# Kernel tuning notes

Measured on AMD Instinct MI355X. Metric: run time of the kernel, lower is better.

The kernel has to match this reference:

```python
import jax, jax.numpy as jnp
import numpy as np

B, C_IN, H, W = 8, 3, 256, 256
CH = 64          # encoder_channels
MSG_LEN = 30     # message_length
WM_R = 4         # watermark_radius
LP_R = 50        # low-pass filter radius


def _wm_positions(h, w, c, r, msg_len):
    # Replicates the nested-loop index ordering of apply_tree_ring_watermark.
    cy, cx = h // 2, w // 2
    ch, rr, cc = [], [], []
    idx = 0
    for chan in range(c):
        for i in range(-r, r + 1):
            for j in range(-r, r + 1):
                if idx >= msg_len:
                    break
                if not (0 <= cy + i < h and 0 <= cx + j < w):
                    continue
                if (i * i + j * j) ** 0.5 <= r:
                    ch.append(chan); rr.append(cy + i); cc.append(cx + j)
                    idx += 1
    return (np.asarray(ch, np.int32), np.asarray(rr, np.int32), np.asarray(cc, np.int32))

_WM_CH, _WM_ROW, _WM_COL = _wm_positions(H, W, CH, WM_R, MSG_LEN)


def conv2d(x, w, b, pad):
    y = jax.lax.conv_general_dilated(x, w, (1, 1), [(pad, pad), (pad, pad)],
                                     dimension_numbers=('NCHW', 'OIHW', 'NCHW'))
    return y + b[None, :, None, None]


def conv_bn_relu(x, w, b, g, be):
    y = conv2d(x, w, b, 1)
    m = y.mean(axis=(0, 2, 3), keepdims=True)
    v = y.var(axis=(0, 2, 3), keepdims=True)
    y = (y - m) * jax.lax.rsqrt(v + 1e-5) * g[None, :, None, None] + be[None, :, None, None]
    return jax.nn.relu(y)


def low_pass_filter(image, radius=LP_R):
    # np.fft per-channel low pass with a circular mask (cv2.circle disk), clip+uint8, /255.
    h, w = image.shape[-2:]
    yy = jnp.arange(h, dtype=jnp.float32) - h // 2
    xx = jnp.arange(w, dtype=jnp.float32) - w // 2
    mask = (yy[:, None] ** 2 + xx[None, :] ** 2) <= float(radius * radius)
    f = jnp.fft.fftshift(jnp.fft.fft2(image), axes=(-2, -1))
    low = jnp.fft.ifft2(jnp.fft.ifftshift(f * mask, axes=(-2, -1))).real
    low = jnp.floor(jnp.clip(low, 0.0, 255.0)) / 255.0  # uint8 cast = floor for non-neg
    # torch version detaches to CPU numpy -> no gradient through this path
    return jax.lax.stop_gradient(low.astype(image.dtype))


def apply_tree_ring_watermark(image_fft, message):
    # Vectorized replacement of the quadruple nested loop: fixed static scatter positions.
    vals = jax.lax.stop_gradient(message).astype(image_fft.dtype) * (1.0 + 1.0j)  # [B, L]
    return image_fft.at[:, _WM_CH, _WM_ROW, _WM_COL].set(vals)


def setup_inputs() -> dict:
    key = jax.random.key(0)
    ks = jax.random.split(key, 8)
    s = 0.05
    return {
        'image': jax.random.uniform(ks[0], (B, C_IN, H, W), jnp.float32) * 255.0,
        'message': jax.random.randint(ks[1], (B, MSG_LEN), 0, 2).astype(jnp.float32),
        'w0': jax.random.normal(ks[2], (CH, C_IN, 3, 3), jnp.float32) * s,
        'b0': jnp.zeros((CH,), jnp.float32),
        'g0': jnp.ones((CH,), jnp.float32),
        'be0': jnp.zeros((CH,), jnp.float32),
        'ws': jax.random.normal(ks[3], (3, CH, CH, 3, 3), jnp.float32) * s,
        'bs': jnp.zeros((3, CH), jnp.float32),
        'gs': jnp.ones((3, CH), jnp.float32),
        'bes': jnp.zeros((3, CH), jnp.float32),
        'acw': jax.random.normal(ks[4], (CH, CH + C_IN + MSG_LEN, 3, 3), jnp.float32) * s,
        'acb': jnp.zeros((CH,), jnp.float32),
        'acg': jnp.ones((CH,), jnp.float32),
        'acbe': jnp.zeros((CH,), jnp.float32),
        'fw': jax.random.normal(ks[5], (3, CH, 1, 1), jnp.float32) * s,
        'fb': jnp.zeros((3,), jnp.float32),
    }


def reference(image, message, w0, b0, g0, be0, ws, bs, gs, bes,
              acw, acb, acg, acbe, fw, fb):
    lp = low_pass_filter(image)
    x = conv_bn_relu(lp, w0, b0, g0, be0)
    for k in range(3):  # encoder_blocks - 1
        x = conv_bn_relu(x, ws[k], bs[k], gs[k], bes[k])
    f = jnp.fft.fft2(x)
    f = apply_tree_ring_watermark(f, message)
    enc = jnp.fft.ifft2(f).real
    msg_exp = jnp.broadcast_to(message[:, :, None, None], (B, MSG_LEN, H, W))
    concat = jnp.concatenate([msg_exp, enc, image], axis=1)
    y = conv_bn_relu(concat, acw, acb, acg, acbe)
    return conv2d(y, fw, fb, 0)
```

## Files before the change

kernel.cpp:

```cpp
#include <hip/hip_runtime.h>
#include <math.h>


#define NPX 65536
typedef unsigned short u16;
typedef __bf16 bfrag_t __attribute__((ext_vector_type(8)));
typedef float f32x4 __attribute__((ext_vector_type(4)));

__constant__ int WM_R_[30] = {124, 125,125,125,125,125, 126,126,126,126,126,126,126,
                              127,127,127,127,127,127,127,
                              128,128,128,128,128,128,128,128,128, 129};
__constant__ int WM_C_[30] = {128, 126,127,128,129,130, 125,126,127,128,129,130,131,
                              125,126,127,128,129,130,131,
                              124,125,126,127,128,129,130,131,132, 125};

__device__ __forceinline__ float bfu2f(unsigned int bits) {
    return __uint_as_float(bits << 16);
}
__device__ __forceinline__ u16 f2bu(float f) {
    unsigned int u = __float_as_uint(f);
    u += 0x7fffu + ((u >> 16) & 1u);
    return (u16)(u >> 16);
}

__global__ void k_tables(float* __restrict__ tw, float* __restrict__ d2t,
                         double* __restrict__ twd64) {
    int idx = blockIdx.x * 256 + threadIdx.x;
    if (idx < 256) {
        double ang = -2.0 * M_PI * (double)idx / 256.0;
        tw[idx]       = (float)cos(ang);
        tw[256 + idx] = (float)sin(ang);
        twd64[idx]       = cos(ang);
        twd64[256 + idx] = sin(ang);
    }
    int q = idx - 256;
    if (q >= 0 && q < 256 * 101) {
        int d = q / 101, kxi = q - d * 101;
        int vx = (kxi <= 50) ? kxi : kxi - 101;
        int r2 = 2500 - vx * vx;
        int L = 0;
        while ((L + 1) * (L + 1) <= r2) L++;
        double s = 1.0;
        for (int v = 1; v <= L; v++) s += 2.0 * cos(2.0 * M_PI * (double)(v * d) / 256.0);
        d2t[kxi * 256 + d] = (float)(s / 256.0);
    }
}

__global__ __launch_bounds__(256) void k_lp1(const float* __restrict__ img,
        const double* __restrict__ twd64, float* __restrict__ Y) {
    __shared__ double rowd[4][256];
    int y0 = blockIdx.x * 4, ch = blockIdx.y, tid = threadIdx.x;
#pragma unroll
    for (int r = 0; r < 4; r++)
        rowd[r][tid] = (double)img[ch * NPX + (y0 + r) * 256 + tid];
    __syncthreads();
    int kxi = tid & 127, rg = tid >> 7;
    if (kxi >= 101) return;
    int kx = (kxi <= 50) ? kxi : kxi + 155;
    double cr = twd64[kx], ci = twd64[256 + kx];
    double wr = 1.0, wi = 0.0;
    double a0r = 0, a0i = 0, a1r = 0, a1i = 0;
    const double* r0 = rowd[2 * rg];
    const double* r1 = rowd[2 * rg + 1];
    for (int x = 0; x < 256; x++) {
        double v0 = r0[x], v1 = r1[x];
        a0r += v0 * wr; a0i += v0 * wi;
        a1r += v1 * wr; a1i += v1 * wi;
        double t = wr * cr - wi * ci;
        wi = wr * ci + wi * cr;
        wr = t;
    }
    int y = y0 + 2 * rg;
    int o = ((kxi * 24 + ch) * 256 + y) * 2;
    Y[o]     = (float)a0r; Y[o + 1] = (float)a0i;
    Y[o + 2] = (float)a1r; Y[o + 3] = (float)a1i;
}

__global__ __launch_bounds__(256) void k_lp2(const float* __restrict__ Y,
        const float* __restrict__ d2t, float* __restrict__ W) {
    __shared__ double Ys[4][256][2];
    __shared__ double Dc[256];
    int kxi = blockIdx.x, chg = blockIdx.y, tid = threadIdx.x;
    const float* src = Y + (size_t)(kxi * 24 + chg * 4) * 512;
    double* ysf = (double*)Ys;
    for (int i = tid; i < 2048; i += 256) ysf[i] = (double)src[i];
    Dc[tid] = (double)d2t[kxi * 256 + tid];
    __syncthreads();
    int cs = tid >> 6, y4 = tid & 63;
    double wr[4] = {0, 0, 0, 0}, wi[4] = {0, 0, 0, 0};
    for (int yp = 0; yp < 256; yp++) {
        double yr = Ys[cs][yp][0], yi = Ys[cs][yp][1];
        double D0 = Dc[(y4 - yp) & 255];
        double D1 = Dc[(y4 + 64 - yp) & 255];
        double D2 = Dc[(y4 + 128 - yp) & 255];
        double D3 = Dc[(y4 + 192 - yp) & 255];
        wr[0] += D0 * yr; wi[0] += D0 * yi;
        wr[1] += D1 * yr; wi[1] += D1 * yi;
        wr[2] += D2 * yr; wi[2] += D2 * yi;
        wr[3] += D3 * yr; wi[3] += D3 * yi;
    }
    int ch = chg * 4 + cs;
#pragma unroll
    for (int k = 0; k < 4; k++) {
        int y = y4 + 64 * k;
        int o = ((ch * 256 + y) * 101 + kxi) * 2;
        W[o] = (float)wr[k]; W[o + 1] = (float)wi[k];
    }
}

__global__ __launch_bounds__(256) void k_lp3(const float* __restrict__ W,
        const double* __restrict__ twd64, float* __restrict__ lp) {
    __shared__ double wsr[101], wsi[101];
    int y = blockIdx.x, ch = blockIdx.y, x = threadIdx.x;
    if (x < 101) {
        int kxi = (x < 50) ? (x + 51) : (x - 50);
        wsr[x] = (double)W[((ch * 256 + y) * 101 + kxi) * 2];
        wsi[x] = (double)W[((ch * 256 + y) * 101 + kxi) * 2 + 1];
    }
    __syncthreads();
    int t0 = (50 * x) & 255;
    double wr = twd64[t0], wi = -twd64[256 + t0];
    double cr = twd64[x], ci = twd64[256 + x];
    double acc = 0.0;
    for (int j = 0; j < 101; j++) {
        acc += wsr[j] * wr + wsi[j] * wi;
        double t = wr * cr - wi * ci;
        wi = wr * ci + wi * cr;
        wr = t;
    }
    acc *= (1.0 / 256.0);
    acc = floor(fmin(fmax(acc, 0.0), 255.0)) / 255.0;
    lp[ch * NPX + y * 256 + x] = (float)acc;
}

__global__ __launch_bounds__(256, 2) void k_conv1(
    const float* __restrict__ lp, const float* __restrict__ w0,
    u16* __restrict__ out) {
    __shared__ float wl[3][9][64];
    __shared__ float al[3][18][18];
    int tid = threadIdx.x;
    int b = blockIdx.z, r0 = blockIdx.y * 16, c0 = blockIdx.x * 16;
    int ocg = tid >> 5, pxg = tid & 31;
    int row = pxg >> 1, chof = (pxg & 1) * 8;
    int oc0 = ocg * 8;
    float acc[8][8];
#pragma unroll
    for (int o = 0; o < 8; o++)
#pragma unroll
        for (int p = 0; p < 8; p++) acc[o][p] = 0.f;
    for (int idx = tid; idx < 1728; idx += 256) {
        int ic = idx / 576, rem = idx - ic * 576;
        int tap = rem >> 6, oc = rem & 63;
        wl[ic][tap][oc] = w0[(oc * 3 + ic) * 9 + tap];
    }
    for (int idx = tid; idx < 972; idx += 256) {
        int ic = idx / 324, rem = idx - ic * 324;
        int ly = rem / 18, lx = rem - ly * 18;
        int gy = r0 - 1 + ly, gx = c0 - 1 + lx;
        float v = 0.f;
        if ((unsigned)gy < 256u && (unsigned)gx < 256u)
            v = lp[(b * 3 + ic) * NPX + gy * 256 + gx];
        al[ic][ly][lx] = v;
    }
    __syncthreads();
    for (int ic = 0; ic < 3; ic++) {
        float areg[3][10];
#pragma unroll
        for (int di = 0; di < 3; di++)
#pragma unroll
            for (int xx = 0; xx < 10; xx++) areg[di][xx] = al[ic][row + di][chof + xx];
#pragma unroll
        for (int tap = 0; tap < 9; tap++) {
            const int di = tap / 3, dj = tap % 3;
            float wv[8];
#pragma unroll
            for (int o = 0; o < 8; o++) wv[o] = wl[ic][tap][oc0 + o];
#pragma unroll
            for (int o = 0; o < 8; o++)
#pragma unroll
                for (int p = 0; p < 8; p++)
                    acc[o][p] = fmaf(wv[o], areg[di][dj + p], acc[o][p]);
        }
    }
#pragma unroll
    for (int p = 0; p < 8; p++) {
        unsigned wd[4];
#pragma unroll
        for (int q = 0; q < 4; q++)
            wd[q] = (unsigned)f2bu(acc[2 * q][p]) | ((unsigned)f2bu(acc[2 * q + 1][p]) << 16);
        size_t addr = ((size_t)((b * 256 + r0 + row) * 256 + c0 + chof + p)) * 64 + oc0;
        uint4 vv; vv.x = wd[0]; vv.y = wd[1]; vv.z = wd[2]; vv.w = wd[3];
        *reinterpret_cast<uint4*>(out + addr) = vv;
    }
}

__global__ void k_wprep(const float* __restrict__ wsv, u16* __restrict__ wp) {
    int bid = blockIdx.x;
    int conv = bid / 72, fg = bid % 72;
    int icc = fg / 36, t2 = fg % 36, tap = t2 / 4, ocb = t2 % 4;
    int l = threadIdx.x;
    int oc = ocb * 16 + (l & 15);
    unsigned wd[4];
#pragma unroll
    for (int q = 0; q < 4; q++) {
        int ic0 = icc * 32 + (l >> 4) * 8 + 2 * q;
        float v0 = wsv[conv * 36864 + (oc * 64 + ic0) * 9 + tap];
        float v1 = wsv[conv * 36864 + (oc * 64 + ic0 + 1) * 9 + tap];
        wd[q] = (unsigned)f2bu(v0) | ((unsigned)f2bu(v1) << 16);
    }
    uint4 vv; vv.x = wd[0]; vv.y = wd[1]; vv.z = wd[2]; vv.w = wd[3];
    reinterpret_cast<uint4*>(wp)[conv * 4608 + fg * 64 + l] = vv;
}

__global__ void k_wprep5(const float* __restrict__ acw, u16* __restrict__ wp5) {
    int fg = blockIdx.x;
    int icc = fg / 36, t2 = fg % 36, tap = t2 / 4, ocb = t2 % 4;
    int l = threadIdx.x;
    int oc = ocb * 16 + (l & 15);
    unsigned wd[4];
#pragma unroll
    for (int q = 0; q < 4; q++) {
        unsigned out2 = 0;
#pragma unroll
        for (int h = 0; h < 2; h++) {
            int icp = icc * 32 + (l >> 4) * 8 + 2 * q + h;
            float v = 0.f;
            if (icp < 67) v = acw[(oc * 97 + 30 + icp) * 9 + tap];
            out2 |= ((unsigned)f2bu(v)) << (16 * h);
        }
        wd[q] = out2;
    }
    uint4 vv; vv.x = wd[0]; vv.y = wd[1]; vv.z = wd[2]; vv.w = wd[3];
    reinterpret_cast<uint4*>(wp5)[fg * 64 + l] = vv;
}

__global__ void k_wsum(const float* __restrict__ acw, float* __restrict__ wsum) {
    for (int e = threadIdx.x; e < 17280; e += 256) {
        int oc = e / 270, r2 = e % 270, ic = r2 / 9, cls = r2 % 9;
        int cy = cls / 3, cx = cls % 3;
        int dil = (cy == 0) ? 1 : 0, dih = (cy == 2) ? 1 : 2;
        int djl = (cx == 0) ? 1 : 0, djh = (cx == 2) ? 1 : 2;
        float s = 0.f;
        for (int di = dil; di <= dih; di++)
            for (int dj = djl; dj <= djh; dj++)
                s += acw[(oc * 97 + ic) * 9 + di * 3 + dj];
        wsum[e] = s;
    }
}

__global__ void k_msgM(const float* __restrict__ msg, const float* __restrict__ wsum,
                       float* __restrict__ M) {
    int b = blockIdx.x;
    for (int t = threadIdx.x; t < 576; t += 256) {
        int oc = t / 9, cls = t % 9;
        float s = 0.f;
        for (int ic = 0; ic < 30; ic++)
            s += msg[b * 30 + ic] * wsum[oc * 270 + ic * 9 + cls];
        M[b * 576 + t] = s;
    }
}

template <int MODE>
__global__ __launch_bounds__(256, 2) void k_cmfma(
    const u16* __restrict__ src, const u16* __restrict__ wp,
    const float* __restrict__ st, const float* __restrict__ img,
    const float* __restrict__ dlt, const float* __restrict__ tw,
    const float* __restrict__ Mterm, u16* __restrict__ out) {
    const int NC = (MODE == 0) ? 2 : 3;
    __shared__ __align__(16) u16 ain[4 * 324 * 8];
    __shared__ float sst[128];
    __shared__ float twl[512];
    __shared__ float dl[60];
    __shared__ float Ml[576];

    int tid = threadIdx.x;
    int wv = tid >> 6, l = tid & 63;
    int b = blockIdx.z, y0 = blockIdx.y * 16, x0 = blockIdx.x * 16;

    if (tid < 128) sst[tid] = st[tid];
    if (MODE == 1) {
        twl[tid] = tw[tid]; twl[tid + 256] = tw[tid + 256];
        if (tid < 60) dl[tid] = dlt[b * 60 + tid];
        for (int i = tid; i < 576; i += 256) Ml[i] = Mterm[b * 576 + i];
    }

    f32x4 acc[4][4];
#pragma unroll
    for (int nt = 0; nt < 4; nt++)
#pragma unroll
        for (int ob = 0; ob < 4; ob++) acc[nt][ob] = (f32x4)(0.f);

    const uint4* wq = reinterpret_cast<const uint4*>(wp);
    const uint4* ap = reinterpret_cast<const uint4*>(ain);
    const int bl = (l >> 4) * 324 + (l & 15);
    const int wv4 = wv * 4;

#pragma unroll 1
    for (int icc = 0; icc < NC; icc++) {
        __syncthreads();
        if (MODE == 1 && icc == 2) {
            for (int i = tid; i < 1296; i += 256) {
                int kb = i / 324, r = i - kb * 324;
                int ly = r / 18, lx = r - ly * 18;
                int gy = y0 - 1 + ly, gx = x0 - 1 + lx;
                uint4 pk; pk.x = 0; pk.y = 0; pk.z = 0; pk.w = 0;
                if (kb == 0 && (unsigned)gy < 256u && (unsigned)gx < 256u) {
                    float v0 = img[(b * 3 + 0) * NPX + gy * 256 + gx];
                    float v1 = img[(b * 3 + 1) * NPX + gy * 256 + gx];
                    float v2 = img[(b * 3 + 2) * NPX + gy * 256 + gx];
                    pk.x = (unsigned)f2bu(v0) | ((unsigned)f2bu(v1) << 16);
                    pk.y = (unsigned)f2bu(v2);
                }
                reinterpret_cast<uint4*>(ain)[i] = pk;
            }
        } else {
            for (int i = tid; i < 1296; i += 256) {
                int kb = i / 324, r = i - kb * 324;
                int ly = r / 18, lx = r - ly * 18;
                int gy = y0 - 1 + ly, gx = x0 - 1 + lx;
                uint4 pk; pk.x = 0; pk.y = 0; pk.z = 0; pk.w = 0;
                if ((unsigned)gy < 256u && (unsigned)gx < 256u) {
                    size_t gaddr = ((size_t)((b * 256 + gy) * 256 + gx)) * 64 + icc * 32 + kb * 8;
                    uint4 u = *reinterpret_cast<const uint4*>(src + gaddr);
                    unsigned wd[4] = {u.x, u.y, u.z, u.w};
                    float f[8];
                    int cb = icc * 32 + kb * 8;
#pragma unroll
                    for (int q = 0; q < 4; q++) {
                        f[2 * q]     = fmaxf(bfu2f(wd[q] & 0xffffu) * sst[2 * (cb + 2 * q)] + sst[2 * (cb + 2 * q) + 1], 0.f);
                        f[2 * q + 1] = fmaxf(bfu2f(wd[q] >> 16)     * sst[2 * (cb + 2 * q + 1)] + sst[2 * (cb + 2 * q + 1) + 1], 0.f);
                    }
                    if (MODE == 1 && icc == 0 && kb == 0) {
                        float corr = 0.f;
#pragma unroll
                        for (int p = 0; p < 30; p++) {
                            int t = (WM_R_[p] * gy + WM_C_[p] * gx) & 255;
                            corr += dl[2 * p] * twl[t] + dl[2 * p + 1] * twl[256 + t];
                        }
                        f[0] += corr * (1.0f / 65536.0f);
                    }
                    unsigned po[4];
#pragma unroll
                    for (int q = 0; q < 4; q++)
                        po[q] = (unsigned)f2bu(f[2 * q]) | ((unsigned)f2bu(f[2 * q + 1]) << 16);
                    pk.x = po[0]; pk.y = po[1]; pk.z = po[2]; pk.w = po[3];
                }
                reinterpret_cast<uint4*>(ain)[i] = pk;
            }
        }
        __syncthreads();

        uint4 a0, a1, a2, a3, n0, n1, n2, n3;
        {
            const uint4* q = wq + ((icc * 9 + 0) * 256 + l);
            a0 = q[0]; a1 = q[64]; a2 = q[128]; a3 = q[192];
        }
#pragma unroll
        for (int tap = 0; tap < 9; tap++) {
            if (tap < 8) {
                const uint4* q = wq + ((icc * 9 + tap + 1) * 256 + l);
                n0 = q[0]; n1 = q[64]; n2 = q[128]; n3 = q[192];
            }
            const int di = tap / 3, dj = tap % 3;
#pragma unroll
            for (int nt = 0; nt < 4; nt++) {
                uint4 braw = ap[bl + (wv4 + nt + di) * 18 + dj];
                bfrag_t bf = __builtin_bit_cast(bfrag_t, braw);
                acc[nt][0] = __builtin_amdgcn_mfma_f32_16x16x32_bf16(
                    __builtin_bit_cast(bfrag_t, a0), bf, acc[nt][0], 0, 0, 0);
                acc[nt][1] = __builtin_amdgcn_mfma_f32_16x16x32_bf16(
                    __builtin_bit_cast(bfrag_t, a1), bf, acc[nt][1], 0, 0, 0);
                acc[nt][2] = __builtin_amdgcn_mfma_f32_16x16x32_bf16(
                    __builtin_bit_cast(bfrag_t, a2), bf, acc[nt][2], 0, 0, 0);
                acc[nt][3] = __builtin_amdgcn_mfma_f32_16x16x32_bf16(
                    __builtin_bit_cast(bfrag_t, a3), bf, acc[nt][3], 0, 0, 0);
            }
            a0 = n0; a1 = n1; a2 = n2; a3 = n3;
        }
    }

    int x = x0 + (l & 15);
    int ocq = (l >> 4) * 4;
    int clsx = (x == 0) ? 0 : ((x == 255) ? 2 : 1);
#pragma unroll
    for (int nt = 0; nt < 4; nt++) {
        int y = y0 + wv4 + nt;
#pragma unroll
        for (int ob = 0; ob < 4; ob++) {
            int oc = ob * 16 + ocq;
            float v0 = acc[nt][ob][0], v1 = acc[nt][ob][1];
            float v2 = acc[nt][ob][2], v3 = acc[nt][ob][3];
            if (MODE == 1) {
                int cls = ((y == 0) ? 0 : ((y == 255) ? 6 : 3)) + clsx;
                v0 += Ml[(oc + 0) * 9 + cls];
                v1 += Ml[(oc + 1) * 9 + cls];
                v2 += Ml[(oc + 2) * 9 + cls];
                v3 += Ml[(oc + 3) * 9 + cls];
            }
            uint2 pk;
            pk.x = (unsigned)f2bu(v0) | ((unsigned)f2bu(v1) << 16);
            pk.y = (unsigned)f2bu(v2) | ((unsigned)f2bu(v3) << 16);
            size_t addr = ((size_t)((b * 256 + y) * 256 + x)) * 64 + oc;
            *reinterpret_cast<uint2*>(out + addr) = pk;
        }
    }
}

__global__ void k_stats(const u16* __restrict__ y, float* __restrict__ part) {
    __shared__ float red[2048];
    int blk = blockIdx.x, tid = threadIdx.x;
    int j = tid & 7, g = tid >> 3;
    float s1[8], s2[8];
#pragma unroll
    for (int k = 0; k < 8; k++) { s1[k] = 0.f; s2[k] = 0.f; }
    for (int it = 0; it < 64; it++) {
        int px = blk * 2048 + it * 32 + g;
        uint4 u = *reinterpret_cast<const uint4*>(y + (size_t)px * 64 + j * 8);
        unsigned wd[4] = {u.x, u.y, u.z, u.w};
#pragma unroll
        for (int q = 0; q < 4; q++) {
            float v0 = bfu2f(wd[q] & 0xffffu), v1 = bfu2f(wd[q] >> 16);
            s1[2 * q] += v0; s2[2 * q] += v0 * v0;
            s1[2 * q + 1] += v1; s2[2 * q + 1] += v1 * v1;
        }
    }
#pragma unroll
    for (int k = 0; k < 8; k++) red[tid * 8 + k] = s1[k];
    __syncthreads();
    if (tid < 64) {
        float a = 0.f;
        for (int gg = 0; gg < 32; gg++) a += red[gg * 64 + tid];
        part[blk * 128 + tid * 2] = a;
    }
    __syncthreads();
#pragma unroll
    for (int k = 0; k < 8; k++) red[tid * 8 + k] = s2[k];
    __syncthreads();
    if (tid < 64) {
        float a = 0.f;
        for (int gg = 0; gg < 32; gg++) a += red[gg * 64 + tid];
        part[blk * 128 + tid * 2 + 1] = a;
    }
}

__global__ void k_finalize(const float* __restrict__ part, const float* __restrict__ g,
                           const float* __restrict__ be, float* __restrict__ st) {
    __shared__ double d1[256], d2[256];
    int tid = threadIdx.x;
    int c = tid >> 2, q = tid & 3;
    double S1 = 0.0, S2 = 0.0;
    for (int k = 0; k < 64; k++) {
        int blk = q * 64 + k;
        S1 += (double)part[blk * 128 + c * 2];
        S2 += (double)part[blk * 128 + c * 2 + 1];
    }
    d1[tid] = S1; d2[tid] = S2;
    __syncthreads();
    if (tid < 64) {
        double T1 = 0.0, T2 = 0.0;
        for (int qq = 0; qq < 4; qq++) { T1 += d1[tid * 4 + qq]; T2 += d2[tid * 4 + qq]; }
        const double Nn = 524288.0;
        double mean = T1 / Nn;
        double var = T2 / Nn - mean * mean;
        float s = (float)((double)g[tid] / sqrt(var + 1e-5));
        float t = (float)((double)be[tid] - mean * (double)s);
        st[tid * 2] = s; st[tid * 2 + 1] = t;
    }
}

__global__ void k_wmG(const u16* __restrict__ y4, const float* __restrict__ st,
                      const float* __restrict__ tw, float* __restrict__ G) {
    __shared__ float twl[512];
    __shared__ float red[256][12];
    int b = blockIdx.x, xg = blockIdx.y, tid = threadIdx.x;
    twl[tid] = tw[tid]; twl[tid + 256] = tw[tid + 256];
    __syncthreads();
    int xs = tid & 31, x = xg * 32 + xs, yg = tid >> 5;
    float s0 = st[0], t0 = st[1];
    float gr[6], gi[6];
#pragma unroll
    for (int r = 0; r < 6; r++) { gr[r] = 0.f; gi[r] = 0.f; }
    for (int yy = 0; yy < 32; yy++) {
        int y = yg * 32 + yy;
        float v = fmaxf(bfu2f((unsigned)y4[((size_t)((b * 256 + y) * 256 + x)) * 64]) * s0 + t0, 0.f);
#pragma unroll
        for (int r = 0; r < 6; r++) {
            int t = ((124 + r) * y) & 255;
            gr[r] += v * twl[t];
            gi[r] += v * twl[256 + t];
        }
    }
#pragma unroll
    for (int r = 0; r < 6; r++) { red[tid][2 * r] = gr[r]; red[tid][2 * r + 1] = gi[r]; }
    __syncthreads();
    for (int e = tid; e < 384; e += 256) {
        int xs2 = e & 31, c = e >> 5;
        float s = 0.f;
        for (int g = 0; g < 8; g++) s += red[g * 32 + xs2][c];
        int r = c >> 1, ri = c & 1;
        G[((b * 6 + r) * 256 + (xg * 32 + xs2)) * 2 + ri] = s;
    }
}

__global__ void k_wmC(const float* __restrict__ G, const float* __restrict__ msg,
                      const float* __restrict__ tw, float* __restrict__ dlt) {
    __shared__ float twl[512];
    __shared__ float fr[256], fi[256];
    int b = blockIdx.x, tid = threadIdx.x;
    twl[tid] = tw[tid]; twl[tid + 256] = tw[tid + 256];
    __syncthreads();
    int p = tid >> 3, part = tid & 7;
    float Fr = 0.f, Fi = 0.f;
    if (p < 30) {
        int rp = WM_R_[p] - 124, c = WM_C_[p];
        for (int xx = part * 32; xx < part * 32 + 32; xx++) {
            float gr = G[((b * 6 + rp) * 256 + xx) * 2];
            float gi = G[((b * 6 + rp) * 256 + xx) * 2 + 1];
            int u = (c * xx) & 255;
            Fr += gr * twl[u] - gi * twl[256 + u];
            Fi += gr * twl[256 + u] + gi * twl[u];
        }
    }
    fr[tid] = Fr; fi[tid] = Fi;
    __syncthreads();
    if (p < 30 && part == 0) {
        float sr = 0.f, si = 0.f;
        for (int k = 0; k < 8; k++) { sr += fr[p * 8 + k]; si += fi[p * 8 + k]; }
        float m = msg[b * 30 + p];
        dlt[b * 60 + p * 2]     = m - sr;
        dlt[b * 60 + p * 2 + 1] = m - si;
    }
}

__global__ void k_final(const u16* __restrict__ y5, const float* __restrict__ st,
                        const float* __restrict__ fw, const float* __restrict__ fb,
                        float* __restrict__ out) {
    __shared__ float fwl[192];
    __shared__ float sl[64], tl[64];
    __shared__ float fbl[3];
    int tid = threadIdx.x;
    if (tid < 192) fwl[tid] = fw[tid];
    if (tid < 64) { sl[tid] = st[tid * 2]; tl[tid] = st[tid * 2 + 1]; }
    if (tid < 3) fbl[tid] = fb[tid];
    __syncthreads();
    int e = blockIdx.x * 256 + tid;
    int b = e >> 16, px = e & 65535;
    float a0 = fbl[0], a1 = fbl[1], a2 = fbl[2];
    const u16* rowp = y5 + (size_t)e * 64;
    for (int cb = 0; cb < 8; cb++) {
        uint4 u = *reinterpret_cast<const uint4*>(rowp + cb * 8);
        unsigned wd[4] = {u.x, u.y, u.z, u.w};
#pragma unroll
        for (int q = 0; q < 4; q++) {
            int c = cb * 8 + 2 * q;
            float v0 = fmaxf(bfu2f(wd[q] & 0xffffu) * sl[c] + tl[c], 0.f);
            float v1 = fmaxf(bfu2f(wd[q] >> 16) * sl[c + 1] + tl[c + 1], 0.f);
            a0 += v0 * fwl[c] + v1 * fwl[c + 1];
            a1 += v0 * fwl[64 + c] + v1 * fwl[64 + c + 1];
            a2 += v0 * fwl[128 + c] + v1 * fwl[128 + c + 1];
        }
    }
    out[(b * 3 + 0) * NPX + px] = a0;
    out[(b * 3 + 1) * NPX + px] = a1;
    out[(b * 3 + 2) * NPX + px] = a2;
}

extern "C" void kernel_launch(void* const* d_in, const int* in_sizes, int n_in,
                              void* d_out, int out_size, void* d_ws, size_t ws_size,
                              hipStream_t stream) {
    (void)in_sizes; (void)n_in; (void)out_size; (void)ws_size;
    const float* image   = (const float*)d_in[0];
    const float* message = (const float*)d_in[1];
    const float* w0      = (const float*)d_in[2];
    const float* g0      = (const float*)d_in[4];
    const float* be0     = (const float*)d_in[5];
    const float* wsv     = (const float*)d_in[6];
    const float* gs      = (const float*)d_in[8];
    const float* bes     = (const float*)d_in[9];
    const float* acw     = (const float*)d_in[10];
    const float* acg     = (const float*)d_in[12];
    const float* acbe    = (const float*)d_in[13];
    const float* fw      = (const float*)d_in[14];
    const float* fb      = (const float*)d_in[15];
    float* out = (float*)d_out;

    u16* XA   = (u16*)d_ws;
    u16* XB   = XA + 33554432;
    float* Yb = (float*)XB;
    float* Wb = Yb + 1241088;
    float* LP = Wb + 1241088;
    u16* WPa  = XB + 33554432;
    u16* WP5  = WPa + 110592;
    float* TW   = (float*)(WP5 + 55296);
    float* D2T  = TW + 512;
    float* PART = D2T + 25856;
    float* ST   = PART + 32768;
    float* DLT  = ST + 128;
    float* G    = DLT + 480;
    float* WSm  = G + 24576;
    float* Mt   = WSm + 17280;
    double* TW64 = (double*)(Mt + 4608);

    dim3 cgrid(16, 16, 8);

    k_tables<<<103, 256, 0, stream>>>(TW, D2T, TW64);
    k_wprep<<<216, 64, 0, stream>>>(wsv, WPa);
    k_wprep5<<<108, 64, 0, stream>>>(acw, WP5);
    k_wsum<<<1, 256, 0, stream>>>(acw, WSm);
    k_msgM<<<8, 256, 0, stream>>>(message, WSm, Mt);

    k_lp1<<<dim3(64, 24), 256, 0, stream>>>(image, TW64, Yb);
    k_lp2<<<dim3(101, 6), 256, 0, stream>>>(Yb, D2T, Wb);
    k_lp3<<<dim3(256, 24), 256, 0, stream>>>(Wb, TW64, LP);

    k_conv1<<<cgrid, 256, 0, stream>>>(LP, w0, XA);
    k_stats<<<256, 256, 0, stream>>>(XA, PART);
    k_finalize<<<1, 256, 0, stream>>>(PART, g0, be0, ST);
    k_cmfma<0><<<cgrid, 256, 0, stream>>>(XA, WPa + 0 * 36864, ST, nullptr, nullptr, nullptr, nullptr, XB);
    k_stats<<<256, 256, 0, stream>>>(XB, PART);
    k_finalize<<<1, 256, 0, stream>>>(PART, gs + 0, bes + 0, ST);
    k_cmfma<0><<<cgrid, 256, 0, stream>>>(XB, WPa + 1 * 36864, ST, nullptr, nullptr, nullptr, nullptr, XA);
    k_stats<<<256, 256, 0, stream>>>(XA, PART);
    k_finalize<<<1, 256, 0, stream>>>(PART, gs + 64, bes + 64, ST);
    k_cmfma<0><<<cgrid, 256, 0, stream>>>(XA, WPa + 2 * 36864, ST, nullptr, nullptr, nullptr, nullptr, XB);
    k_stats<<<256, 256, 0, stream>>>(XB, PART);
    k_finalize<<<1, 256, 0, stream>>>(PART, gs + 128, bes + 128, ST);
    k_wmG<<<dim3(8, 8), 256, 0, stream>>>(XB, ST, TW, G);
    k_wmC<<<8, 256, 0, stream>>>(G, message, TW, DLT);
    k_cmfma<1><<<cgrid, 256, 0, stream>>>(XB, WP5, ST, image, DLT, TW, Mt, XA);
    k_stats<<<256, 256, 0, stream>>>(XA, PART);
    k_finalize<<<1, 256, 0, stream>>>(PART, acg, acbe, ST);
    k_final<<<2048, 256, 0, stream>>>(XA, ST, fw, fb, out);
}
```

Before: 731.7 us.

## Stage all input channels in LDS once and flatten MFMA conv loop

The MFMA conv kernel now loads the full halo tile for all input-channel chunks into shared memory in one pass, using per-pixel 128-byte loads, instead of reloading per 32-channel chunk with a sync pair each time. The tap loop becomes one flat loop over chunk and tap with the weights for the next step prefetched. Float-to-bf16 packing now uses the hardware v_cvt_pk_bf16_f32 instruction, and launch bounds are raised to 3 blocks per SM. LDS use grows a lot, to about 41KB for MODE 0 and 62KB for MODE 1, which may cap occupancy and pressure registers. The hardware conversion may also round NaN and other edge cases differently from the old software rounding.

```diff
diff --git a/kernel.cpp b/kernel.cpp
--- a/kernel.cpp
+++ b/kernel.cpp
@@ -21,6 +21,11 @@
     unsigned int u = __float_as_uint(f);
     u += 0x7fffu + ((u >> 16) & 1u);
     return (u16)(u >> 16);
+}
+__device__ __forceinline__ unsigned cvt_pk(float lo, float hi) {
+    unsigned r;
+    asm("v_cvt_pk_bf16_f32 %0, %1, %2" : "=v"(r) : "v"(lo), "v"(hi));
+    return r;
 }
 
 __global__ void k_tables(float* __restrict__ tw, float* __restrict__ d2t,
@@ -187,7 +192,7 @@
         unsigned wd[4];
 #pragma unroll
         for (int q = 0; q < 4; q++)
-            wd[q] = (unsigned)f2bu(acc[2 * q][p]) | ((unsigned)f2bu(acc[2 * q + 1][p]) << 16);
+            wd[q] = cvt_pk(acc[2 * q][p], acc[2 * q + 1][p]);
         size_t addr = ((size_t)((b * 256 + r0 + row) * 256 + c0 + chof + p)) * 64 + oc0;
         uint4 vv; vv.x = wd[0]; vv.y = wd[1]; vv.z = wd[2]; vv.w = wd[3];
         *reinterpret_cast<uint4*>(out + addr) = vv;
@@ -261,17 +266,17 @@
 }
 
 template <int MODE>
-__global__ __launch_bounds__(256, 2) void k_cmfma(
+__global__ __launch_bounds__(256, 3) void k_cmfma(
     const u16* __restrict__ src, const u16* __restrict__ wp,
     const float* __restrict__ st, const float* __restrict__ img,
     const float* __restrict__ dlt, const float* __restrict__ tw,
     const float* __restrict__ Mterm, u16* __restrict__ out) {
-    const int NC = (MODE == 0) ? 2 : 3;
-    __shared__ __align__(16) u16 ain[4 * 324 * 8];
+    const int NKB = (MODE == 0) ? 8 : 12;
+    __shared__ __align__(16) u16 ain[NKB * 324 * 8];
     __shared__ float sst[128];
-    __shared__ float twl[512];
-    __shared__ float dl[60];
-    __shared__ float Ml[576];
+    __shared__ float twl[(MODE == 1) ? 512 : 1];
+    __shared__ float dl[(MODE == 1) ? 60 : 1];
+    __shared__ float Ml[(MODE == 1) ? 576 : 1];
 
     int tid = threadIdx.x;
     int wv = tid >> 6, l = tid & 63;
@@ -283,6 +288,62 @@
         if (tid < 60) dl[tid] = dlt[b * 60 + tid];
         for (int i = tid; i < 576; i += 256) Ml[i] = Mterm[b * 576 + i];
     }
+    __syncthreads();
+
+    for (int px = tid; px < 324; px += 256) {
+        int ly = px / 18, lx = px - ly * 18;
+        int gy = y0 - 1 + ly, gx = x0 - 1 + lx;
+        bool inb = ((unsigned)gy < 256u) && ((unsigned)gx < 256u);
+        uint4* dst = reinterpret_cast<uint4*>(ain) + px;
+        const uint4* gp = nullptr;
+        if (inb) gp = reinterpret_cast<const uint4*>(
+            src + ((size_t)((b * 256 + gy) * 256 + gx)) * 64);
+        float corr = 0.f;
+        if (MODE == 1) {
+            if (inb) {
+#pragma unroll
+                for (int p = 0; p < 30; p++) {
+                    int t = (WM_R_[p] * gy + WM_C_[p] * gx) & 255;
+                    corr += dl[2 * p] * twl[t] + dl[2 * p + 1] * twl[256 + t];
+                }
+                corr *= (1.0f / 65536.0f);
+            }
+        }
+#pragma unroll
+        for (int kb = 0; kb < 8; kb++) {
+            uint4 pk; pk.x = 0; pk.y = 0; pk.z = 0; pk.w = 0;
+            if (inb) {
+                uint4 u = gp[kb];
+                int cb = kb * 8;
+                float f0 = fmaxf(bfu2f(u.x & 0xffffu) * sst[2 * cb + 0]  + sst[2 * cb + 1],  0.f);
+                float f1 = fmaxf(bfu2f(u.x >> 16)     * sst[2 * cb + 2]  + sst[2 * cb + 3],  0.f);
+                float f2 = fmaxf(bfu2f(u.y & 0xffffu) * sst[2 * cb + 4]  + sst[2 * cb + 5],  0.f);
+                float f3 = fmaxf(bfu2f(u.y >> 16)     * sst[2 * cb + 6]  + sst[2 * cb + 7],  0.f);
+                float f4 = fmaxf(bfu2f(u.z & 0xffffu) * sst[2 * cb + 8]  + sst[2 * cb + 9],  0.f);
+                float f5 = fmaxf(bfu2f(u.z >> 16)     * sst[2 * cb + 10] + sst[2 * cb + 11], 0.f);
+                float f6 = fmaxf(bfu2f(u.w & 0xffffu) * sst[2 * cb + 12] + sst[2 * cb + 13], 0.f);
+                float f7 = fmaxf(bfu2f(u.w >> 16)     * sst[2 * cb + 14] + sst[2 * cb + 15], 0.f);
+                if (MODE == 1 && kb == 0) f0 += corr;
+                pk.x = cvt_pk(f0, f1); pk.y = cvt_pk(f2, f3);
+                pk.z = cvt_pk(f4, f5); pk.w = cvt_pk(f6, f7);
+            }
+            dst[kb * 324] = pk;
+        }
+        if (MODE == 1) {
+            uint4 p8; p8.x = 0; p8.y = 0; p8.z = 0; p8.w = 0;
+            if (inb) {
+                float v0 = img[(b * 3 + 0) * NPX + gy * 256 + gx];
+                float v1 = img[(b * 3 + 1) * NPX + gy * 256 + gx];
+                float v2 = img[(b * 3 + 2) * NPX + gy * 256 + gx];
+                p8.x = cvt_pk(v0, v1);
+                p8.y = cvt_pk(v2, 0.f);
+            }
+            dst[8 * 324] = p8;
+            uint4 z; z.x = 0; z.y = 0; z.z = 0; z.w = 0;
+            dst[9 * 324] = z; dst[10 * 324] = z; dst[11 * 324] = z;
+        }
+    }
+    __syncthreads();
 
     f32x4 acc[4][4];
 #pragma unroll
@@ -294,89 +355,33 @@
     const uint4* ap = reinterpret_cast<const uint4*>(ain);
     const int bl = (l >> 4) * 324 + (l & 15);
     const int wv4 = wv * 4;
-
+    const int NIT = (NKB / 4) * 9;
+
+    uint4 a0 = wq[l], a1 = wq[64 + l], a2 = wq[128 + l], a3 = wq[192 + l];
 #pragma unroll 1
-    for (int icc = 0; icc < NC; icc++) {
-        __syncthreads();
-        if (MODE == 1 && icc == 2) {
-            for (int i = tid; i < 1296; i += 256) {
-                int kb = i / 324, r = i - kb * 324;
-                int ly = r / 18, lx = r - ly * 18;
-                int gy = y0 - 1 + ly, gx = x0 - 1 + lx;
-                uint4 pk; pk.x = 0; pk.y = 0; pk.z = 0; pk.w = 0;
-                if (kb == 0 && (unsigned)gy < 256u && (unsigned)gx < 256u) {
-                    float v0 = img[(b * 3 + 0) * NPX + gy * 256 + gx];
-                    float v1 = img[(b * 3 + 1) * NPX + gy * 256 + gx];
-                    float v2 = img[(b * 3 + 2) * NPX + gy * 256 + gx];
-                    pk.x = (unsigned)f2bu(v0) | ((unsigned)f2bu(v1) << 16);
-                    pk.y = (unsigned)f2bu(v2);
-                }
-                reinterpret_cast<uint4*>(ain)[i] = pk;
-            }
-        } else {
-            for (int i = tid; i < 1296; i += 256) {
-                int kb = i / 324, r = i - kb * 324;
-                int ly = r / 18, lx = r - ly * 18;
-                int gy = y0 - 1 + ly, gx = x0 - 1 + lx;
-                uint4 pk; pk.x = 0; pk.y = 0; pk.z = 0; pk.w = 0;
-                if ((unsigned)gy < 256u && (unsigned)gx < 256u) {
-                    size_t gaddr = ((size_t)((b * 256 + gy) * 256 + gx)) * 64 + icc * 32 + kb * 8;
-                    uint4 u = *reinterpret_cast<const uint4*>(src + gaddr);
-                    unsigned wd[4] = {u.x, u.y, u.z, u.w};
-                    float f[8];
-                    int cb = icc * 32 + kb * 8;
-#pragma unroll
-                    for (int q = 0; q < 4; q++) {
-                        f[2 * q]     = fmaxf(bfu2f(wd[q] & 0xffffu) * sst[2 * (cb + 2 * q)] + sst[2 * (cb + 2 * q) + 1], 0.f);
-                        f[2 * q + 1] = fmaxf(bfu2f(wd[q] >> 16)     * sst[2 * (cb + 2 * q + 1)] + sst[2 * (cb + 2 * q + 1) + 1], 0.f);
-                    }
-                    if (MODE == 1 && icc == 0 && kb == 0) {
-                        float corr = 0.f;
-#pragma unroll
-                        for (int p = 0; p < 30; p++) {
-                            int t = (WM_R_[p] * gy + WM_C_[p] * gx) & 255;
-                            corr += dl[2 * p] * twl[t] + dl[2 * p + 1] * twl[256 + t];
-                        }
-                        f[0] += corr * (1.0f / 65536.0f);
-                    }
-                    unsigned po[4];
-#pragma unroll
-                    for (int q = 0; q < 4; q++)
-                        po[q] = (unsigned)f2bu(f[2 * q]) | ((unsigned)f2bu(f[2 * q + 1]) << 16);
-                    pk.x = po[0]; pk.y = po[1]; pk.z = po[2]; pk.w = po[3];
-                }
-                reinterpret_cast<uint4*>(ain)[i] = pk;
-            }
-        }
-        __syncthreads();
-
-        uint4 a0, a1, a2, a3, n0, n1, n2, n3;
-        {
-            const uint4* q = wq + ((icc * 9 + 0) * 256 + l);
-            a0 = q[0]; a1 = q[64]; a2 = q[128]; a3 = q[192];
-        }
-#pragma unroll
-        for (int tap = 0; tap < 9; tap++) {
-            if (tap < 8) {
-                const uint4* q = wq + ((icc * 9 + tap + 1) * 256 + l);
-                n0 = q[0]; n1 = q[64]; n2 = q[128]; n3 = q[192];
-            }
-            const int di = tap / 3, dj = tap % 3;
-#pragma unroll
-            for (int nt = 0; nt < 4; nt++) {
-                uint4 braw = ap[bl + (wv4 + nt + di) * 18 + dj];
-                bfrag_t bf = __builtin_bit_cast(bfrag_t, braw);
-                acc[nt][0] = __builtin_amdgcn_mfma_f32_16x16x32_bf16(
-                    __builtin_bit_cast(bfrag_t, a0), bf, acc[nt][0], 0, 0, 0);
-                acc[nt][1] = __builtin_amdgcn_mfma_f32_16x16x32_bf16(
-                    __builtin_bit_cast(bfrag_t, a1), bf, acc[nt][1], 0, 0, 0);
-                acc[nt][2] = __builtin_amdgcn_mfma_f32_16x16x32_bf16(
-                    __builtin_bit_cast(bfrag_t, a2), bf, acc[nt][2], 0, 0, 0);
-                acc[nt][3] = __builtin_amdgcn_mfma_f32_16x16x32_bf16(
-                    __builtin_bit_cast(bfrag_t, a3), bf, acc[nt][3], 0, 0, 0);
-            }
-            a0 = n0; a1 = n1; a2 = n2; a3 = n3;
-        }
+    for (int it = 0; it < NIT; it++) {
+        uint4 n0, n1, n2, n3;
+        if (it + 1 < NIT) {
+            const uint4* q = wq + (it + 1) * 256 + l;
+            n0 = q[0]; n1 = q[64]; n2 = q[128]; n3 = q[192];
+        }
+        int icc = it / 9, tap = it - icc * 9;
+        int di = tap / 3, dj = tap - di * 3;
+        int abase = icc * 4 * 324 + bl + dj;
+#pragma unroll
+        for (int nt = 0; nt < 4; nt++) {
+            uint4 braw = ap[abase + (wv4 + nt + di) * 18];
+            bfrag_t bf = __builtin_bit_cast(bfrag_t, braw);
+            acc[nt][0] = __builtin_amdgcn_mfma_f32_16x16x32_bf16(
+                __builtin_bit_cast(bfrag_t, a0), bf, acc[nt][0], 0, 0, 0);
+            acc[nt][1] = __builtin_amdgcn_mfma_f32_16x16x32_bf16(
+                __builtin_bit_cast(bfrag_t, a1), bf, acc[nt][1], 0, 0, 0);
+            acc[nt][2] = __builtin_amdgcn_mfma_f32_16x16x32_bf16(
+                __builtin_bit_cast(bfrag_t, a2), bf, acc[nt][2], 0, 0, 0);
+            acc[nt][3] = __builtin_amdgcn_mfma_f32_16x16x32_bf16(
+                __builtin_bit_cast(bfrag_t, a3), bf, acc[nt][3], 0, 0, 0);
+        }
+        a0 = n0; a1 = n1; a2 = n2; a3 = n3;
     }
 
     int x = x0 + (l & 15);
@@ -398,8 +403,8 @@
                 v3 += Ml[(oc + 3) * 9 + cls];
             }
             uint2 pk;
-            pk.x = (unsigned)f2bu(v0) | ((unsigned)f2bu(v1) << 16);
-            pk.y = (unsigned)f2bu(v2) | ((unsigned)f2bu(v3) << 16);
+            pk.x = cvt_pk(v0, v1);
+            pk.y = cvt_pk(v2, v3);
             size_t addr = ((size_t)((b * 256 + y) * 256 + x)) * 64 + oc;
             *reinterpret_cast<uint2*>(out + addr) = pk;
         }
```

Result: slower. 752.4 us (+2.8%).
